# Optimization experiments

Measured on AMD Instinct MI355X. Metric: run time of the kernel, lower is better.

The kernel has to match this reference:

```python
import jax, jax.numpy as jnp
import numpy as np

NEG_SLOPE = 0.2  # PyG GATConv default negative_slope
N_NODES = 10000
N_EDGES = 320000
IN_CH = 512
HID = 128
HEADS = 4
N_CLASSES = 2


def gat_conv(x, src, dst, n, W, att_src, att_dst, bias, concat):
    """PyG-style GATConv (shared weights for src/dst, eval mode: no dropout)."""
    H, C = att_src.shape
    h = (x @ W).reshape(-1, H, C)                      # [N, H, C]
    a_src = jnp.sum(h * att_src[None], axis=-1)        # [N, H]
    a_dst = jnp.sum(h * att_dst[None], axis=-1)        # [N, H]
    e = a_src[src] + a_dst[dst]                        # [E, H]
    e = jnp.where(e > 0, e, NEG_SLOPE * e)             # LeakyReLU
    # numerically stable softmax over incoming edges of each dst node
    m = jax.ops.segment_max(e, dst, num_segments=n)    # [N, H]
    m = jnp.where(jnp.isfinite(m), m, 0.0)
    ex = jnp.exp(e - m[dst])
    denom = jax.ops.segment_sum(ex, dst, num_segments=n)
    alpha = ex / (denom[dst] + 1e-16)                  # [E, H]
    out = jax.ops.segment_sum(alpha[:, :, None] * h[src], dst, num_segments=n)  # [N,H,C]
    if concat:
        out = out.reshape(n, H * C)
    else:
        out = out.mean(axis=1)
    return out + bias


def setup_inputs() -> dict:
    key = jax.random.key(0)
    ks = jax.random.split(key, 8)
    x = jax.random.normal(ks[0], (N_NODES, IN_CH), dtype=jnp.float32)
    edge_index = jax.random.randint(ks[1], (2, N_EDGES), 0, N_NODES, dtype=jnp.int32)
    s1 = 1.0 / np.sqrt(IN_CH)
    s2 = 1.0 / np.sqrt(HEADS * HID)
    return {
        "x": x,
        "edge_index": edge_index,
        "W1": jax.random.normal(ks[2], (IN_CH, HEADS * HID), dtype=jnp.float32) * s1,
        "att_src1": jax.random.normal(ks[3], (HEADS, HID), dtype=jnp.float32) * s2,
        "att_dst1": jax.random.normal(ks[4], (HEADS, HID), dtype=jnp.float32) * s2,
        "b1": jnp.zeros((HEADS * HID,), dtype=jnp.float32),
        "W2": jax.random.normal(ks[5], (HEADS * HID, N_CLASSES), dtype=jnp.float32) * s2,
        "att_src2": jax.random.normal(ks[6], (1, N_CLASSES), dtype=jnp.float32),
        "att_dst2": jax.random.normal(ks[7], (1, N_CLASSES), dtype=jnp.float32),
        "b2": jnp.zeros((N_CLASSES,), dtype=jnp.float32),
    }


def reference(x, edge_index, W1, att_src1, att_dst1, b1, W2, att_src2, att_dst2, b2):
    n = x.shape[0]
    loop = jnp.arange(n, dtype=edge_index.dtype)       # PyG add_self_loops=True
    src = jnp.concatenate([edge_index[0], loop])
    dst = jnp.concatenate([edge_index[1], loop])
    h = gat_conv(x, src, dst, n, W1, att_src1, att_dst1, b1, concat=True)
    h = jax.nn.elu(h)
    out = gat_conv(h, src, dst, n, W2, att_src2, att_dst2, b2, concat=False)
    return out
```

## Files before the change

kernel.cpp:

```cpp
#include <hip/hip_runtime.h>
#include <hip/hip_bf16.h>

#define N_NODES 10000
#define N_EDGES 320000
#define E_TOT   330000
#define IN_CH   512
#define F1      512
#define HID     128
#define HEADS   4
#define SLOTS   128

typedef __attribute__((ext_vector_type(8))) short bf16x8;
typedef __attribute__((ext_vector_type(4))) float f32x4;

__device__ __forceinline__ float lo16(unsigned u) { return __uint_as_float(u << 16); }
__device__ __forceinline__ float hi16(unsigned u) { return __uint_as_float(u & 0xffff0000u); }
__device__ __forceinline__ unsigned short bfbits(float f) {
    __hip_bfloat16 h = __float2bfloat16(f);
    return *(unsigned short*)&h;
}

__global__ void k_prep(const float* __restrict__ x, unsigned short* __restrict__ xb,
                       const float* __restrict__ w1, __hip_bfloat16* __restrict__ w1t,
                       int* __restrict__ zbase) {
    int b = blockIdx.x;
    if (b < 5000) {
        int idx = b * 256 + threadIdx.x;
        float4 v = ((const float4*)x)[idx];
        ushort4 u;
        u.x = bfbits(v.x); u.y = bfbits(v.y); u.z = bfbits(v.z); u.w = bfbits(v.w);
        ((ushort4*)xb)[idx] = u;
    } else if (b < 6024) {
        int idx = (b - 5000) * 256 + threadIdx.x;
        int k = idx >> 9, n = idx & 511;
        w1t[(size_t)n * 512 + k] = __float2bfloat16(w1[idx]);
    } else {
        int idx = (b - 6024) * 256 + threadIdx.x;
        if (idx < 90000) zbase[idx] = 0;
    }
}

__global__ __launch_bounds__(256) void k_gemm1(const __hip_bfloat16* __restrict__ xb,
                                               const __hip_bfloat16* __restrict__ w1t,
                                               const float* __restrict__ as_vec,
                                               const float* __restrict__ ad_vec,
                                               __hip_bfloat16* __restrict__ h1b,
                                               float* __restrict__ a_src,
                                               float* __restrict__ a_dst) {
    int wid = blockIdx.x * 4 + (threadIdx.x >> 6);
    int lane = threadIdx.x & 63;
    int tm = wid >> 3, tn = wid & 7;
    int col16 = lane & 15, quad = lane >> 4;
    int klo = quad * 8;
    int r0g = tm * 32;
    const __hip_bfloat16* a0p = xb + (size_t)min(r0g + col16, N_NODES - 1) * IN_CH + klo;
    const __hip_bfloat16* a1p = xb + (size_t)min(r0g + 16 + col16, N_NODES - 1) * IN_CH + klo;
    const __hip_bfloat16* bp  = w1t + (size_t)(tn * 64 + col16) * IN_CH + klo;
    f32x4 acc[2][4] = {};
    for (int kt = 0; kt < IN_CH; kt += 32) {
        bf16x8 a0 = *(const bf16x8*)(a0p + kt);
        bf16x8 a1 = *(const bf16x8*)(a1p + kt);
#pragma unroll
        for (int ct = 0; ct < 4; ++ct) {
            bf16x8 b = *(const bf16x8*)(bp + (size_t)(ct * 16) * IN_CH + kt);
            acc[0][ct] = __builtin_amdgcn_mfma_f32_16x16x32_bf16(a0, b, acc[0][ct], 0, 0, 0);
            acc[1][ct] = __builtin_amdgcn_mfma_f32_16x16x32_bf16(a1, b, acc[1][ct], 0, 0, 0);
        }
    }
    int h_w = tn >> 1;
    float asv[4], adv[4];
#pragma unroll
    for (int ct = 0; ct < 4; ++ct) {
        int c = tn * 64 + ct * 16 + col16;
        asv[ct] = as_vec[c];
        adv[ct] = ad_vec[c];
    }
#pragma unroll
    for (int rt = 0; rt < 2; ++rt) {
#pragma unroll
        for (int reg = 0; reg < 4; ++reg) {
            int row = r0g + rt * 16 + quad * 4 + reg;
            float ps = 0.f, pd = 0.f;
            bool ok = row < N_NODES;
#pragma unroll
            for (int ct = 0; ct < 4; ++ct) {
                float v = acc[rt][ct][reg];
                ps += v * asv[ct];
                pd += v * adv[ct];
                if (ok) h1b[(size_t)row * F1 + tn * 64 + ct * 16 + col16] = __float2bfloat16(v);
            }
#pragma unroll
            for (int off = 1; off <= 8; off <<= 1) {
                ps += __shfl_xor(ps, off);
                pd += __shfl_xor(pd, off);
            }
            if (col16 == 0 && ok) {
                atomicAdd(&a_src[row * HEADS + h_w], ps);
                atomicAdd(&a_dst[row * HEADS + h_w], pd);
            }
        }
    }
}

__global__ void k_place(const int* __restrict__ src, const int* __restrict__ dst,
                        int* __restrict__ cnt, int* __restrict__ slots) {
    int e = blockIdx.x * 256 + threadIdx.x;
    if (e >= E_TOT) return;
    int d, s;
    if (e < N_EDGES) { d = dst[e]; s = src[e]; } else { d = e - N_EDGES; s = d; }
    int pos = atomicAdd(&cnt[d], 1);
    if (pos < SLOTS) slots[d * SLOTS + pos] = s;
}

__global__ __launch_bounds__(256) void k_aggr1(const __hip_bfloat16* __restrict__ h1b,
                                               const float* __restrict__ a_src,
                                               const float* __restrict__ a_dst,
                                               const int* __restrict__ cnt,
                                               const int* __restrict__ slots,
                                               const float* __restrict__ b1,
                                               const float* __restrict__ w2,
                                               const float* __restrict__ as2,
                                               const float* __restrict__ ad2,
                                               float* __restrict__ h2,
                                               float* __restrict__ a_src2,
                                               float* __restrict__ a_dst2) {
    int n = blockIdx.x * 4 + (threadIdx.x >> 6);
    int lane = threadIdx.x & 63;
    int h = lane >> 4;
    int cn = min(cnt[n], SLOTS);
    const int* sl = slots + n * SLOTS;
    float adst = a_dst[n * HEADS + h];
    float dsum = 0.f;
    float acc[8] = {};
    const __hip_bfloat16* hb = h1b + lane * 8;
    int i = 0;
    for (; i + 8 <= cn; i += 8) {
        int s[8];
        uint4 d[8];
        float w[8];
#pragma unroll
        for (int j = 0; j < 8; ++j) s[j] = sl[i + j];
#pragma unroll
        for (int j = 0; j < 8; ++j) d[j] = *(const uint4*)(hb + (size_t)s[j] * F1);
#pragma unroll
        for (int j = 0; j < 8; ++j) {
            float e = a_src[s[j] * HEADS + h] + adst;
            e = fmaxf(e, 0.2f * e);
            w[j] = __expf(e);
            dsum += w[j];
        }
#pragma unroll
        for (int j = 0; j < 8; ++j) {
            acc[0] += w[j] * lo16(d[j].x); acc[1] += w[j] * hi16(d[j].x);
            acc[2] += w[j] * lo16(d[j].y); acc[3] += w[j] * hi16(d[j].y);
            acc[4] += w[j] * lo16(d[j].z); acc[5] += w[j] * hi16(d[j].z);
            acc[6] += w[j] * lo16(d[j].w); acc[7] += w[j] * hi16(d[j].w);
        }
    }
    for (; i < cn; ++i) {
        int s = sl[i];
        uint4 dv = *(const uint4*)(hb + (size_t)s * F1);
        float e = a_src[s * HEADS + h] + adst;
        e = fmaxf(e, 0.2f * e);
        float w = __expf(e);
        dsum += w;
        acc[0] += w * lo16(dv.x); acc[1] += w * hi16(dv.x);
        acc[2] += w * lo16(dv.y); acc[3] += w * hi16(dv.y);
        acc[4] += w * lo16(dv.z); acc[5] += w * hi16(dv.z);
        acc[6] += w * lo16(dv.w); acc[7] += w * hi16(dv.w);
    }
    float inv = 1.f / (dsum + 1e-16f);
    int c0 = lane * 8;
    float ps0 = 0.f, ps1 = 0.f;
#pragma unroll
    for (int j = 0; j < 8; ++j) {
        float v = acc[j] * inv + b1[c0 + j];
        v = v > 0.f ? v : __expf(v) - 1.f;
        ps0 += v * w2[(c0 + j) * 2 + 0];
        ps1 += v * w2[(c0 + j) * 2 + 1];
    }
#pragma unroll
    for (int off = 1; off <= 32; off <<= 1) {
        ps0 += __shfl_xor(ps0, off);
        ps1 += __shfl_xor(ps1, off);
    }
    if (lane == 0) {
        h2[n * 2 + 0] = ps0;
        h2[n * 2 + 1] = ps1;
        a_src2[n] = ps0 * as2[0] + ps1 * as2[1];
        a_dst2[n] = ps0 * ad2[0] + ps1 * ad2[1];
    }
}

__global__ __launch_bounds__(256) void k_aggr2(const float* __restrict__ h2,
                                               const float* __restrict__ a_src2,
                                               const float* __restrict__ a_dst2,
                                               const int* __restrict__ cnt,
                                               const int* __restrict__ slots,
                                               const float* __restrict__ b2,
                                               float* __restrict__ out) {
    int lane = threadIdx.x & 63;
    int sub = lane >> 4, slot = lane & 15;
    int n = blockIdx.x * 16 + (threadIdx.x >> 6) * 4 + sub;
    int cn = min(cnt[n], SLOTS);
    const int* sl = slots + n * SLOTS;
    float adst = a_dst2[n];
    float dsum = 0.f, acc0 = 0.f, acc1 = 0.f;
    for (int i = slot; i < cn; i += 16) {
        int s = sl[i];
        float e = a_src2[s] + adst;
        e = fmaxf(e, 0.2f * e);
        float w = __expf(e);
        dsum += w;
        acc0 += w * h2[s * 2 + 0];
        acc1 += w * h2[s * 2 + 1];
    }
#pragma unroll
    for (int off = 1; off <= 8; off <<= 1) {
        dsum += __shfl_xor(dsum, off);
        acc0 += __shfl_xor(acc0, off);
        acc1 += __shfl_xor(acc1, off);
    }
    if (slot == 0) {
        float inv = 1.f / (dsum + 1e-16f);
        out[n * 2 + 0] = acc0 * inv + b2[0];
        out[n * 2 + 1] = acc1 * inv + b2[1];
    }
}

extern "C" void kernel_launch(void* const* d_in, const int* in_sizes, int n_in,
                              void* d_out, int out_size, void* d_ws, size_t ws_size,
                              hipStream_t stream) {
    const float* x   = (const float*)d_in[0];
    const int*   ei  = (const int*)d_in[1];
    const float* W1  = (const float*)d_in[2];
    const float* as1 = (const float*)d_in[3];
    const float* ad1 = (const float*)d_in[4];
    const float* b1  = (const float*)d_in[5];
    const float* W2  = (const float*)d_in[6];
    const float* as2 = (const float*)d_in[7];
    const float* ad2 = (const float*)d_in[8];
    const float* b2  = (const float*)d_in[9];

    char* ws = (char*)d_ws;
    __hip_bfloat16* h1b = (__hip_bfloat16*)(ws);
    __hip_bfloat16* xb  = (__hip_bfloat16*)(ws + 10240000);
    __hip_bfloat16* w1t = (__hip_bfloat16*)(ws + 20480000);
    const size_t S = 21004288;
    float* a_src1 = (float*)(ws + S);
    float* a_dst1 = (float*)(ws + S + 160000);
    int*   cnt    = (int*)(ws + S + 320000);
    int*   slots  = (int*)(ws + S + 360000);
    float* h2     = (float*)(ws + S + 5480000);
    float* a_src2 = (float*)(ws + S + 5560000);
    float* a_dst2 = (float*)(ws + S + 5600000);

    const int* srcArr = ei;
    const int* dstArr = ei + N_EDGES;

    k_prep<<<5000 + 1024 + 352, 256, 0, stream>>>(x, (unsigned short*)xb, W1, w1t,
                                                  (int*)a_src1);
    k_place<<<(E_TOT + 255) / 256, 256, 0, stream>>>(srcArr, dstArr, cnt, slots);
    k_gemm1<<<626, 256, 0, stream>>>(xb, w1t, as1, ad1, h1b, a_src1, a_dst1);
    k_aggr1<<<N_NODES / 4, 256, 0, stream>>>(h1b, a_src1, a_dst1, cnt, slots, b1,
                                             W2, as2, ad2, h2, a_src2, a_dst2);
    k_aggr2<<<N_NODES / 16, 256, 0, stream>>>(h2, a_src2, a_dst2, cnt, slots, b2,
                                              (float*)d_out);
}
```

Measured before the change: 191.5 us.

## Fuse edge placement into prep kernel, tile W1 transpose, prefetch GEMM loads

Edge slot placement now runs inside the prep kernel, and cnt is zeroed by a separate memset, which removes one kernel launch. The W1 transpose goes through a shared-memory tile so both its reads and writes are coalesced, replacing the strided scatter. The GEMM K-loop is unrolled and double-buffers its A/B register fragments, so the loads for the next step are issued before the current MFMAs. This costs extra registers and adds a memset launch. The zero range shrinks from 90000 to 80000 ints, since cnt is now cleared separately.

```diff
diff --git a/kernel.cpp b/kernel.cpp
--- a/kernel.cpp
+++ b/kernel.cpp
@@ -21,22 +21,45 @@
 }
 
 __global__ void k_prep(const float* __restrict__ x, unsigned short* __restrict__ xb,
-                       const float* __restrict__ w1, __hip_bfloat16* __restrict__ w1t,
-                       int* __restrict__ zbase) {
+                       const float* __restrict__ w1, unsigned short* __restrict__ w1t,
+                       int* __restrict__ zbase,
+                       const int* __restrict__ src, const int* __restrict__ dst,
+                       int* __restrict__ cnt, int* __restrict__ slots) {
+    __shared__ float tile[64][65];
     int b = blockIdx.x;
+    int t = threadIdx.x;
     if (b < 5000) {
-        int idx = b * 256 + threadIdx.x;
+        int idx = b * 256 + t;
         float4 v = ((const float4*)x)[idx];
         ushort4 u;
         u.x = bfbits(v.x); u.y = bfbits(v.y); u.z = bfbits(v.z); u.w = bfbits(v.w);
         ((ushort4*)xb)[idx] = u;
-    } else if (b < 6024) {
-        int idx = (b - 5000) * 256 + threadIdx.x;
-        int k = idx >> 9, n = idx & 511;
-        w1t[(size_t)n * 512 + k] = __float2bfloat16(w1[idx]);
+    } else if (b < 5064) {
+        int bb = b - 5000;
+        int bi = bb >> 3, bj = bb & 7;
+        int r0 = t >> 6, col = t & 63;
+#pragma unroll
+        for (int p = 0; p < 16; ++p) {
+            int row = p * 4 + r0;
+            tile[row][col] = w1[(size_t)(bi * 64 + row) * 512 + bj * 64 + col];
+        }
+        __syncthreads();
+#pragma unroll
+        for (int p = 0; p < 16; ++p) {
+            int row = p * 4 + r0;
+            w1t[(size_t)(bj * 64 + row) * 512 + bi * 64 + col] = bfbits(tile[col][row]);
+        }
+    } else if (b < 5377) {
+        int idx = (b - 5064) * 256 + t;
+        if (idx < 80000) zbase[idx] = 0;
     } else {
-        int idx = (b - 6024) * 256 + threadIdx.x;
-        if (idx < 90000) zbase[idx] = 0;
+        int e = (b - 5377) * 256 + t;
+        if (e < E_TOT) {
+            int d, s;
+            if (e < N_EDGES) { d = dst[e]; s = src[e]; } else { d = e - N_EDGES; s = d; }
+            int pos = atomicAdd(&cnt[d], 1);
+            if (pos < SLOTS) slots[d * SLOTS + pos] = s;
+        }
     }
 }
 
@@ -57,14 +80,30 @@
     const __hip_bfloat16* a1p = xb + (size_t)min(r0g + 16 + col16, N_NODES - 1) * IN_CH + klo;
     const __hip_bfloat16* bp  = w1t + (size_t)(tn * 64 + col16) * IN_CH + klo;
     f32x4 acc[2][4] = {};
+    bf16x8 a0c = *(const bf16x8*)(a0p);
+    bf16x8 a1c = *(const bf16x8*)(a1p);
+    bf16x8 bc[4];
+#pragma unroll
+    for (int ct = 0; ct < 4; ++ct) bc[ct] = *(const bf16x8*)(bp + (size_t)(ct * 16) * IN_CH);
+#pragma unroll
     for (int kt = 0; kt < IN_CH; kt += 32) {
-        bf16x8 a0 = *(const bf16x8*)(a0p + kt);
-        bf16x8 a1 = *(const bf16x8*)(a1p + kt);
+        bf16x8 a0n, a1n, bn[4];
+        if (kt + 32 < IN_CH) {
+            a0n = *(const bf16x8*)(a0p + kt + 32);
+            a1n = *(const bf16x8*)(a1p + kt + 32);
+#pragma unroll
+            for (int ct = 0; ct < 4; ++ct)
+                bn[ct] = *(const bf16x8*)(bp + (size_t)(ct * 16) * IN_CH + kt + 32);
+        }
 #pragma unroll
         for (int ct = 0; ct < 4; ++ct) {
-            bf16x8 b = *(const bf16x8*)(bp + (size_t)(ct * 16) * IN_CH + kt);
-            acc[0][ct] = __builtin_amdgcn_mfma_f32_16x16x32_bf16(a0, b, acc[0][ct], 0, 0, 0);
-            acc[1][ct] = __builtin_amdgcn_mfma_f32_16x16x32_bf16(a1, b, acc[1][ct], 0, 0, 0);
+            acc[0][ct] = __builtin_amdgcn_mfma_f32_16x16x32_bf16(a0c, bc[ct], acc[0][ct], 0, 0, 0);
+            acc[1][ct] = __builtin_amdgcn_mfma_f32_16x16x32_bf16(a1c, bc[ct], acc[1][ct], 0, 0, 0);
+        }
+        if (kt + 32 < IN_CH) {
+            a0c = a0n; a1c = a1n;
+#pragma unroll
+            for (int ct = 0; ct < 4; ++ct) bc[ct] = bn[ct];
         }
     }
     int h_w = tn >> 1;
@@ -100,16 +139,6 @@
             }
         }
     }
-}
-
-__global__ void k_place(const int* __restrict__ src, const int* __restrict__ dst,
-                        int* __restrict__ cnt, int* __restrict__ slots) {
-    int e = blockIdx.x * 256 + threadIdx.x;
-    if (e >= E_TOT) return;
-    int d, s;
-    if (e < N_EDGES) { d = dst[e]; s = src[e]; } else { d = e - N_EDGES; s = d; }
-    int pos = atomicAdd(&cnt[d], 1);
-    if (pos < SLOTS) slots[d * SLOTS + pos] = s;
 }
 
 __global__ __launch_bounds__(256) void k_aggr1(const __hip_bfloat16* __restrict__ h1b,
@@ -258,9 +287,10 @@
     const int* srcArr = ei;
     const int* dstArr = ei + N_EDGES;
 
-    k_prep<<<5000 + 1024 + 352, 256, 0, stream>>>(x, (unsigned short*)xb, W1, w1t,
-                                                  (int*)a_src1);
-    k_place<<<(E_TOT + 255) / 256, 256, 0, stream>>>(srcArr, dstArr, cnt, slots);
+    hipMemsetAsync(cnt, 0, N_NODES * sizeof(int), stream);
+    k_prep<<<5377 + 1290, 256, 0, stream>>>(x, (unsigned short*)xb, W1,
+                                            (unsigned short*)w1t, (int*)a_src1,
+                                            srcArr, dstArr, cnt, slots);
     k_gemm1<<<626, 256, 0, stream>>>(xb, w1t, as1, ad1, h1b, a_src1, a_dst1);
     k_aggr1<<<N_NODES / 4, 256, 0, stream>>>(h1b, a_src1, a_dst1, cnt, slots, b1,
                                              W2, as2, ad2, h2, a_src2, a_dst2);
```

New measurement: 189.7 us. No clear change (-1.0%).
